# Performance work log

Measured on AMD Instinct MI355X. Metric: run time of the kernel, lower is better.

## Reference

```python
import jax, jax.numpy as jnp
import numpy as np

N, IN, OUT, RANK = 8192, 4096, 4096, 256

def setup_inputs() -> dict:
    key = jax.random.key(0)
    ks = jax.random.split(key, 7)
    x = jax.random.normal(ks[0], (N, IN), dtype=jnp.float32)
    # original frozen linear layer params
    W = jax.random.normal(ks[1], (OUT, IN), dtype=jnp.float32) * (1.0 / np.sqrt(IN))
    bias = jax.random.normal(ks[2], (OUT,), dtype=jnp.float32) * 0.01
    # frozen shared low-rank matrices (kaiming-uniform-like scale)
    A_frozen = jax.random.normal(ks[3], (RANK, IN), dtype=jnp.float32) * (1.0 / np.sqrt(IN))
    B_frozen = jax.random.normal(ks[4], (OUT, RANK), dtype=jnp.float32) * (1.0 / np.sqrt(RANK))
    # trainable VeRA vectors (b_vec is zeros at init; use small randn so delta is nonzero)
    b_vec = jax.random.normal(ks[5], (OUT,), dtype=jnp.float32) * 0.01
    d_vec = jnp.full((RANK,), 0.1, dtype=jnp.float32) + jax.random.normal(ks[6], (RANK,), dtype=jnp.float32) * 0.01
    return {"x": x, "W": W, "bias": bias, "A_frozen": A_frozen, "B_frozen": B_frozen, "b_vec": b_vec, "d_vec": d_vec}

def reference(x, W, bias, A_frozen, B_frozen, b_vec, d_vec):
    # original frozen linear: [N, OUT]
    orig = x @ W.T + bias
    # diag(b) @ B @ diag(d) @ A @ x.T  ==  (((x @ A.T) * d) @ B.T) * b, transposed
    h = (x @ A_frozen.T) * d_vec            # [N, RANK]
    delta = (h @ B_frozen.T) * b_vec        # [N, OUT]
    return orig + delta
```

## Files before the change

kernel.cpp:

```cpp
#include <hip/hip_runtime.h>

#define IN_DIM 4096
#define OUT_DIM 4096
#define N_ROWS 8192
#define RANK 256

typedef __bf16 bf16x8 __attribute__((ext_vector_type(8)));
typedef float f32x4 __attribute__((ext_vector_type(4)));
typedef unsigned short u16;
typedef unsigned short u16x4 __attribute__((ext_vector_type(4)));

__device__ __forceinline__ u16 f2b(float f) {
    unsigned int u = __builtin_bit_cast(unsigned int, f);
    unsigned int r = u + 0x7FFFu + ((u >> 16) & 1u);
    return (u16)(r >> 16);
}

__device__ __forceinline__ void async16(const void* g, const void* l) {
    __builtin_amdgcn_global_load_lds(
        (const __attribute__((address_space(1))) void*)g,
        (__attribute__((address_space(3))) void*)l, 16, 0, 0);
}

__global__ __launch_bounds__(256) void cvt4(const float* __restrict__ s,
                                            u16* __restrict__ d, int n4) {
    int i = blockIdx.x * 256 + threadIdx.x;
    if (i >= n4) return;
    f32x4 v = __builtin_nontemporal_load((const f32x4*)s + i);
    u16x4 o;
    o.x = f2b(v.x); o.y = f2b(v.y); o.z = f2b(v.z); o.w = f2b(v.w);
    *((u16x4*)d + i) = o;
}

__global__ __launch_bounds__(256) void vera_adt(const float* __restrict__ A,
                                                const float* __restrict__ d,
                                                u16* __restrict__ adt) {
    int r = threadIdx.x;
    int i0 = blockIdx.x * 64;
    float dv = d[r];
    const float* ap = A + (size_t)r * IN_DIM + i0;
#pragma unroll 4
    for (int j = 0; j < 64; ++j)
        adt[(size_t)(i0 + j) * RANK + r] = f2b(__builtin_nontemporal_load(ap + j) * dv);
}

template <int MODE, int K, int NN, int TM, int TN>
__global__ __launch_bounds__(256) void vera_gemm(
    const u16* __restrict__ Aop, const u16* __restrict__ Bop,
    const float* __restrict__ W, const float* __restrict__ bvec,
    void* __restrict__ outv) {
    __shared__ __align__(16) __bf16 As[128 * 32];
    __shared__ __align__(16) __bf16 Bs[128 * 32];

    const int tid = threadIdx.x;
    const int lane = tid & 63;
    const int wavei = __builtin_amdgcn_readfirstlane(tid >> 6);
    const int fr = lane & 15;
    const int fq = lane >> 4;
    const int wm = (wavei >> 1) * 64;
    const int wn = (wavei & 1) * 64;

    constexpr int G = 8;
    const int bid = blockIdx.x;
    const int g = bid / (G * TN);
    const int r = bid - g * (G * TN);
    const int bm = (g * G + (r & (G - 1))) * 128;
    const int bn = (r / G) * 128;

    const int srow = tid >> 2;
    const int sk = (tid & 3) * 8;
    const u16* ga0 = Aop + (size_t)(bm + srow) * K + sk;
    const u16* ga1 = Aop + (size_t)(bm + 64 + srow) * K + sk;
    const u16* gb0 = Bop + (size_t)(bn + srow) * K + sk;
    const u16* gb1 = Bop + (size_t)(bn + 64 + srow) * K + sk;

    char* lAs = (char*)As;
    char* lBs = (char*)Bs;
    const int lo = wavei * 1024;

    f32x4 acc[4][4] = {};

    for (int k0 = 0; k0 < K; k0 += 32) {
        __syncthreads();
        async16(ga0 + k0, lAs + lo);
        async16(ga1 + k0, lAs + 4096 + lo);
        async16(gb0 + k0, lBs + lo);
        async16(gb1 + k0, lBs + 4096 + lo);
        __syncthreads();

        const __bf16* ap = As + (wm + fr) * 32 + fq * 8;
        const __bf16* bp = Bs + (wn + fr) * 32 + fq * 8;
        bf16x8 af[4], bfr[4];
#pragma unroll
        for (int i = 0; i < 4; ++i) {
            af[i] = *(const bf16x8*)(ap + i * 16 * 32);
            bfr[i] = *(const bf16x8*)(bp + i * 16 * 32);
        }
#pragma unroll
        for (int mi = 0; mi < 4; ++mi)
#pragma unroll
            for (int ni = 0; ni < 4; ++ni)
                acc[mi][ni] = __builtin_amdgcn_mfma_f32_16x16x32_bf16(
                    af[mi], bfr[ni], acc[mi][ni], 0, 0, 0);
    }

#pragma unroll
    for (int ni = 0; ni < 4; ++ni) {
        const int col = bn + wn + ni * 16 + fr;
        float bcol = (MODE == 1) ? bvec[col] : 0.f;
#pragma unroll
        for (int mi = 0; mi < 4; ++mi) {
            const int row0 = bm + wm + mi * 16 + fq * 4;
#pragma unroll
            for (int v = 0; v < 4; ++v) {
                const int row = row0 + v;
                float a = acc[mi][ni][v];
                if (MODE == 0) {
                    float wv = __builtin_nontemporal_load(&W[(size_t)row * NN + col]);
                    ((u16*)outv)[(size_t)row * NN + col] = f2b(wv + bvec[row] * a);
                } else {
                    __builtin_nontemporal_store(a + bcol,
                        &((float*)outv)[(size_t)row * NN + col]);
                }
            }
        }
    }
}

#define BARW() do { __builtin_amdgcn_s_barrier(); \
    asm volatile("s_waitcnt lgkmcnt(0)" ::: "memory"); \
    __builtin_amdgcn_sched_barrier(0); } while (0)
#define W6()   asm volatile("s_waitcnt vmcnt(6)" ::: "memory")
#define ENDP() __builtin_amdgcn_s_barrier()

template <int K, int MT, int NTL>
__global__ __launch_bounds__(512, 2) void gemm256(
    const u16* __restrict__ Aop, const u16* __restrict__ Bop,
    const float* __restrict__ bvec, float* __restrict__ out) {
    constexpr int NTK = K / 64;
    __shared__ __align__(16) char lds[131072];
    char* const L = (char*)lds;

    const int tid = threadIdx.x;
    const int lane = tid & 63;
    const int wavei = __builtin_amdgcn_readfirstlane(tid >> 6);
    const int fr = lane & 15;
    const int fq = lane >> 4;
    const int wmi = wavei >> 2;
    const int wni = wavei & 3;

    constexpr int NWG = MT * NTL;
    const int bid = blockIdx.x;
    const int idx = (bid & 7) * (NWG / 8) + (bid >> 3);
    const int bm = (idx % MT) * 256;
    const int bn = (idx / MT) * 256;

    const int c0 = wavei * 128 + lane;
    const int r0 = c0 >> 2;
    const int k0of = ((c0 & 3) ^ ((r0 >> 1) & 3)) * 8;
    const int c1 = c0 + 64;
    const int r1 = c1 >> 2;
    const int k1of = ((c1 & 3) ^ ((r1 >> 1) & 3)) * 8;
    const u16* gA0 = Aop + (size_t)(bm + r0) * K + k0of;
    const u16* gA1 = Aop + (size_t)(bm + r1) * K + k1of;
    const u16* gB0 = Bop + (size_t)(bn + r0) * K + k0of;
    const u16* gB1 = Bop + (size_t)(bn + r1) * K + k1of;
    const int wl = wavei * 2048;

    auto stageA = [&](int tau, int j, int slot) {
        const int kb = tau * 64 + j * 32;
        async16(gA0 + kb, L + slot * 16384 + wl);
        async16(gA1 + kb, L + slot * 16384 + wl + 1024);
    };
    auto stageB = [&](int tau, int j, int slot) {
        const int kb = tau * 64 + j * 32;
        async16(gB0 + kb, L + 65536 + slot * 16384 + wl);
        async16(gB1 + kb, L + 65536 + slot * 16384 + wl + 1024);
    };

    const int aswz = ((fq ^ ((fr >> 1) & 3)) << 4);
    const int aoff = (wmi * 128 + fr) * 64 + aswz;
    const int boff = 65536 + (wni * 64 + fr) * 64 + aswz;

    bf16x8 af[4], bf[4];
    f32x4 acc[8][4] = {};

    auto ldA = [&](int slot, int mh) {
        const char* p = L + slot * 16384 + aoff + mh * 4096;
#pragma unroll
        for (int i = 0; i < 4; ++i) af[i] = *(const bf16x8*)(p + i * 1024);
    };
    auto ldB = [&](int slot) {
        const char* p = L + slot * 16384 + boff;
#pragma unroll
        for (int i = 0; i < 4; ++i) bf[i] = *(const bf16x8*)(p + i * 1024);
    };
    auto MF = [&](int mh) {
        __builtin_amdgcn_s_setprio(1);
#pragma unroll
        for (int mi = 0; mi < 4; ++mi)
#pragma unroll
            for (int ni = 0; ni < 4; ++ni)
                acc[mh * 4 + mi][ni] = __builtin_amdgcn_mfma_f32_16x16x32_bf16(
                    af[mi], bf[ni], acc[mh * 4 + mi][ni], 0, 0, 0);
        __builtin_amdgcn_s_setprio(0);
    };

    stageA(0, 0, 0); stageB(0, 0, 0);
    stageA(0, 1, 1); stageB(0, 1, 1);
    stageA(1, 0, 2);
    asm volatile("s_waitcnt vmcnt(6)" ::: "memory");
    __builtin_amdgcn_s_barrier();

#pragma unroll 1
    for (int it = 0; it < NTK / 2; ++it) {
        const int t  = 2 * it;
        const int t1 = t + 1;
        const int t2 = (t + 2 < NTK) ? t + 2 : NTK - 1;
        const int t3 = (t + 3 < NTK) ? t + 3 : NTK - 1;

        ldA(0, 0); ldB(0); stageB(t1, 0, 2); BARW(); MF(0); ENDP();
        ldA(0, 1);         stageA(t1, 1, 3); BARW(); MF(1); W6(); ENDP();
        ldA(1, 0); ldB(1); stageB(t1, 1, 3); BARW(); MF(0); ENDP();
        ldA(1, 1);         stageA(t2, 0, 0); BARW(); MF(1); W6(); ENDP();
        ldA(2, 0); ldB(2); stageB(t2, 0, 0); BARW(); MF(0); ENDP();
        ldA(2, 1);         stageA(t2, 1, 1); BARW(); MF(1); W6(); ENDP();
        ldA(3, 0); ldB(3); stageB(t2, 1, 1); BARW(); MF(0); ENDP();
        ldA(3, 1);         stageA(t3, 0, 2); BARW(); MF(1); W6(); ENDP();
    }

    asm volatile("s_waitcnt vmcnt(0)" ::: "memory");

    const int colb = bn + wni * 64 + fr;
    const int rowb = bm + wmi * 128 + fq * 4;
#pragma unroll
    for (int ni = 0; ni < 4; ++ni) {
        const int col = colb + ni * 16;
        const float bc = bvec[col];
#pragma unroll
        for (int m8 = 0; m8 < 8; ++m8) {
            const int row = rowb + (m8 >> 2) * 64 + (m8 & 3) * 16;
#pragma unroll
            for (int v = 0; v < 4; ++v)
                __builtin_nontemporal_store(acc[m8][ni][v] + bc,
                    &out[(size_t)(row + v) * (NTL * 256) + col]);
        }
    }
}

extern "C" void kernel_launch(void* const* d_in, const int* in_sizes, int n_in,
                              void* d_out, int out_size, void* d_ws, size_t ws_size,
                              hipStream_t stream) {
    (void)in_sizes; (void)n_in; (void)out_size; (void)ws_size;
    const float* x    = (const float*)d_in[0];
    const float* W    = (const float*)d_in[1];
    const float* bias = (const float*)d_in[2];
    const float* A    = (const float*)d_in[3];
    const float* B    = (const float*)d_in[4];
    const float* bv   = (const float*)d_in[5];
    const float* dv   = (const float*)d_in[6];

    char* ws = (char*)d_ws;
    u16* xb  = (u16*)ws;
    u16* wb  = (u16*)(ws + (size_t)N_ROWS * IN_DIM * 2);
    u16* adt = (u16*)(ws + (size_t)N_ROWS * IN_DIM * 2
                         + (size_t)OUT_DIM * IN_DIM * 2);
    u16* Bb  = adt + (size_t)IN_DIM * RANK;

    cvt4<<<dim3(OUT_DIM * RANK / 4 / 256), 256, 0, stream>>>(B, Bb, OUT_DIM * RANK / 4);
    vera_adt<<<dim3(IN_DIM / 64), 256, 0, stream>>>(A, dv, adt);
    vera_gemm<0, RANK, IN_DIM, OUT_DIM / 128, IN_DIM / 128>
        <<<dim3((OUT_DIM / 128) * (IN_DIM / 128)), 256, 0, stream>>>(
        Bb, adt, W, bv, wb);
    cvt4<<<dim3(N_ROWS * IN_DIM / 4 / 256), 256, 0, stream>>>(x, xb, N_ROWS * IN_DIM / 4);
    gemm256<IN_DIM, N_ROWS / 256, OUT_DIM / 256>
        <<<dim3((N_ROWS / 256) * (OUT_DIM / 256)), 512, 0, stream>>>(
        xb, wb, bias, (float*)d_out);
}
```

Measured before the change: 542.2 us.

## Stage weight-merge epilogue through LDS for coalesced loads and stores; reorder tile mapping

The merged-weight GEMM epilogue now writes the accumulator tile to shared memory as bf16, then reads it back row-contiguously. Each thread loads eight W floats as vectors and writes eight bf16 outputs at once, replacing per-element strided global accesses. The main GEMM's block-to-tile mapping is switched so consecutive tiles walk along N instead of M, which changes L2 reuse. The epilogue rounds the low-rank product to bf16 before adding it to W, a small extra precision loss, and adds an LDS round trip and barriers.

```diff
diff --git a/kernel.cpp b/kernel.cpp
--- a/kernel.cpp
+++ b/kernel.cpp
@@ -9,11 +9,16 @@
 typedef float f32x4 __attribute__((ext_vector_type(4)));
 typedef unsigned short u16;
 typedef unsigned short u16x4 __attribute__((ext_vector_type(4)));
+typedef unsigned short u16x8 __attribute__((ext_vector_type(8)));
 
 __device__ __forceinline__ u16 f2b(float f) {
     unsigned int u = __builtin_bit_cast(unsigned int, f);
     unsigned int r = u + 0x7FFFu + ((u >> 16) & 1u);
     return (u16)(r >> 16);
+}
+
+__device__ __forceinline__ float b2f(u16 s) {
+    return __builtin_bit_cast(float, (unsigned int)s << 16);
 }
 
 __device__ __forceinline__ void async16(const void* g, const void* l) {
@@ -44,13 +49,14 @@
         adt[(size_t)(i0 + j) * RANK + r] = f2b(__builtin_nontemporal_load(ap + j) * dv);
 }
 
-template <int MODE, int K, int NN, int TM, int TN>
+template <int K, int NN, int TM, int TN>
 __global__ __launch_bounds__(256) void vera_gemm(
     const u16* __restrict__ Aop, const u16* __restrict__ Bop,
     const float* __restrict__ W, const float* __restrict__ bvec,
-    void* __restrict__ outv) {
-    __shared__ __align__(16) __bf16 As[128 * 32];
-    __shared__ __align__(16) __bf16 Bs[128 * 32];
+    u16* __restrict__ outv) {
+    __shared__ __align__(16) char smem[32768];
+    __bf16* As = (__bf16*)smem;
+    __bf16* Bs = (__bf16*)(smem + 8192);
 
     const int tid = threadIdx.x;
     const int lane = tid & 63;
@@ -104,26 +110,42 @@
                     af[mi], bfr[ni], acc[mi][ni], 0, 0, 0);
     }
 
+    __syncthreads();
+    u16* S = (u16*)smem;
 #pragma unroll
     for (int ni = 0; ni < 4; ++ni) {
-        const int col = bn + wn + ni * 16 + fr;
-        float bcol = (MODE == 1) ? bvec[col] : 0.f;
+        const int cl = wn + ni * 16 + fr;
 #pragma unroll
         for (int mi = 0; mi < 4; ++mi) {
-            const int row0 = bm + wm + mi * 16 + fq * 4;
 #pragma unroll
             for (int v = 0; v < 4; ++v) {
-                const int row = row0 + v;
-                float a = acc[mi][ni][v];
-                if (MODE == 0) {
-                    float wv = __builtin_nontemporal_load(&W[(size_t)row * NN + col]);
-                    ((u16*)outv)[(size_t)row * NN + col] = f2b(wv + bvec[row] * a);
-                } else {
-                    __builtin_nontemporal_store(a + bcol,
-                        &((float*)outv)[(size_t)row * NN + col]);
-                }
+                const int rl = wm + mi * 16 + fq * 4 + v;
+                S[rl * 128 + cl] = f2b(acc[mi][ni][v]);
             }
         }
+    }
+    __syncthreads();
+#pragma unroll
+    for (int j = 0; j < 8; ++j) {
+        const int c = tid + j * 256;
+        const int rl = c >> 4;
+        const int cl = (c & 15) * 8;
+        const int grow = bm + rl;
+        const size_t goff = (size_t)grow * NN + (bn + cl);
+        u16x8 sv = *(const u16x8*)(S + rl * 128 + cl);
+        f32x4 w0 = __builtin_nontemporal_load((const f32x4*)(W + goff));
+        f32x4 w1 = __builtin_nontemporal_load((const f32x4*)(W + goff + 4));
+        const float bvr = bvec[grow];
+        u16x8 o;
+        o[0] = f2b(w0.x + bvr * b2f(sv[0]));
+        o[1] = f2b(w0.y + bvr * b2f(sv[1]));
+        o[2] = f2b(w0.z + bvr * b2f(sv[2]));
+        o[3] = f2b(w0.w + bvr * b2f(sv[3]));
+        o[4] = f2b(w1.x + bvr * b2f(sv[4]));
+        o[5] = f2b(w1.y + bvr * b2f(sv[5]));
+        o[6] = f2b(w1.z + bvr * b2f(sv[6]));
+        o[7] = f2b(w1.w + bvr * b2f(sv[7]));
+        *(u16x8*)(outv + goff) = o;
     }
 }
 
@@ -152,8 +174,8 @@
     constexpr int NWG = MT * NTL;
     const int bid = blockIdx.x;
     const int idx = (bid & 7) * (NWG / 8) + (bid >> 3);
-    const int bm = (idx % MT) * 256;
-    const int bn = (idx / MT) * 256;
+    const int bn = (idx % NTL) * 256;
+    const int bm = (idx / NTL) * 256;
 
     const int c0 = wavei * 128 + lane;
     const int r0 = c0 >> 2;
@@ -214,10 +236,9 @@
 
 #pragma unroll 1
     for (int it = 0; it < NTK / 2; ++it) {
-        const int t  = 2 * it;
-        const int t1 = t + 1;
-        const int t2 = (t + 2 < NTK) ? t + 2 : NTK - 1;
-        const int t3 = (t + 3 < NTK) ? t + 3 : NTK - 1;
+        const int t1 = 2 * it + 1;
+        const int t2 = (2 * it + 2 < NTK) ? 2 * it + 2 : NTK - 1;
+        const int t3 = (2 * it + 3 < NTK) ? 2 * it + 3 : NTK - 1;
 
         ldA(0, 0); ldB(0); stageB(t1, 0, 2); BARW(); MF(0); ENDP();
         ldA(0, 1);         stageA(t1, 1, 3); BARW(); MF(1); W6(); ENDP();
@@ -269,7 +290,7 @@
 
     cvt4<<<dim3(OUT_DIM * RANK / 4 / 256), 256, 0, stream>>>(B, Bb, OUT_DIM * RANK / 4);
     vera_adt<<<dim3(IN_DIM / 64), 256, 0, stream>>>(A, dv, adt);
-    vera_gemm<0, RANK, IN_DIM, OUT_DIM / 128, IN_DIM / 128>
+    vera_gemm<RANK, IN_DIM, OUT_DIM / 128, IN_DIM / 128>
         <<<dim3((OUT_DIM / 128) * (IN_DIM / 128)), 256, 0, stream>>>(
         Bb, adt, W, bv, wb);
     cvt4<<<dim3(N_ROWS * IN_DIM / 4 / 256), 256, 0, stream>>>(x, xb, N_ROWS * IN_DIM / 4);
```

Measured after the change: 505.4 us. 1.07x faster.
